# Kernel tuning notes

Measured on AMD Instinct MI355X. Metric: run time of the kernel, lower is better.

Reference implementation:

```python
import jax, jax.numpy as jnp
import numpy as np

N_HEADS = 8
WINDOW = 4

def setup_inputs() -> dict:
    key = jax.random.key(0)
    ks = jax.random.split(key, 12)
    B, C, L = 8, 512, 1024
    Dh = C // N_HEADS
    s = 1.0 / np.sqrt(C)
    inp = {
        'x': jax.random.normal(ks[0], (B, C, L), dtype=jnp.float32),
        'Wq': jax.random.normal(ks[1], (C, C), dtype=jnp.float32) * s,
        'bq': jnp.zeros((C,), dtype=jnp.float32),
        'Wk': jax.random.normal(ks[2], (C, C), dtype=jnp.float32) * s,
        'bk': jnp.zeros((C,), dtype=jnp.float32),
        'Wv': jax.random.normal(ks[3], (C, C), dtype=jnp.float32) * s,
        'bv': jnp.zeros((C,), dtype=jnp.float32),
        'Wo': jax.random.normal(ks[4], (C, C), dtype=jnp.float32) * s,
        'bo': jnp.zeros((C,), dtype=jnp.float32),
        'emb_rel_k': jax.random.normal(ks[5], (2 * WINDOW + 1, Dh), dtype=jnp.float32) * 0.02,
        'emb_rel_v': jax.random.normal(ks[6], (2 * WINDOW + 1, Dh), dtype=jnp.float32) * 0.02,
    }
    return inp


def reference(x, Wq, bq, Wk, bk, Wv, bv, Wo, bo, emb_rel_k, emb_rel_v):
    B, C, L = x.shape
    H = N_HEADS
    Dh = C // H
    scale = Dh ** -0.5

    def proj(W, b):
        # pointwise conv1d == channel-mixing matmul; (B,C,L) -> (B,H,L,Dh)
        y = jnp.einsum('oc,bcl->bol', W, x) + b[:, None]
        return y.reshape(B, H, Dh, L).transpose(0, 1, 3, 2)

    q = proj(Wq, bq) * scale
    k = proj(Wk, bk)
    v = proj(Wv, bv)

    scores = jnp.einsum('bhld,bhjd->bhlj', q, k)  # (B,H,L,L)

    t = jnp.arange(L)
    diff = t[None, :] - t[:, None]                      # (L,L)
    window_mask = (jnp.abs(diff) <= WINDOW)
    indices = jnp.clip(diff, -WINDOW, WINDOW) + WINDOW  # (L,L) in [0, 2w]

    rel_k = emb_rel_k[indices]                          # (L,L,Dh)
    rel_scores = jnp.einsum('bhld,ljd->bhlj', q, rel_k)
    scores = scores + rel_scores * window_mask[None, None, :, :]

    attn = jax.nn.softmax(scores, axis=-1)

    out = jnp.einsum('bhlj,bhjd->bhld', attn, v)
    rel_v = emb_rel_v[indices] * window_mask[:, :, None]  # (L,L,Dh)
    out = out + jnp.einsum('bhlj,ljd->bhld', attn, rel_v)

    out = out.transpose(0, 1, 3, 2).reshape(B, C, L)
    out = jnp.einsum('oc,bcl->bol', Wo, out) + bo[:, None]
    return out
```

## Files before the change

### kernel.cpp

```cpp
#include <hip/hip_runtime.h>
#include <math.h>

#define B_  8
#define H_  8
#define C_  512
#define L_  1024
#define DH  64
#define WIN 4

typedef __attribute__((ext_vector_type(8))) short short8;
typedef __attribute__((ext_vector_type(4))) float floatx4;

__device__ __forceinline__ unsigned short f2bf(float f) {
    unsigned int u = __float_as_uint(f);
    u = u + 0x7FFFu + ((u >> 16) & 1u);
    return (unsigned short)(u >> 16);
}
__device__ __forceinline__ float bf2f(unsigned short h) {
    return __uint_as_float(((unsigned int)h) << 16);
}
__device__ __forceinline__ unsigned short f2h(float f) {
    _Float16 h = (_Float16)f;
    return *reinterpret_cast<unsigned short*>(&h);
}

__global__ __launch_bounds__(256) void prep_kernel(
    const float* __restrict__ Wq, const float* __restrict__ Wk,
    const float* __restrict__ Wv, const float* __restrict__ Wo,
    const float* __restrict__ bq, const float* __restrict__ bk,
    const float* __restrict__ bv,
    unsigned short* __restrict__ Wqkv_hi,
    unsigned short* __restrict__ Wo_h,
    float* __restrict__ bqkv)
{
    const int i = blockIdx.x * 256 + threadIdx.x;
    float4 v; ushort4 h;

    v = ((const float4*)Wq)[i];
    h.x = f2bf(v.x); h.y = f2bf(v.y); h.z = f2bf(v.z); h.w = f2bf(v.w);
    ((ushort4*)Wqkv_hi)[i] = h;

    v = ((const float4*)Wk)[i];
    h.x = f2bf(v.x); h.y = f2bf(v.y); h.z = f2bf(v.z); h.w = f2bf(v.w);
    ((ushort4*)Wqkv_hi)[65536 + i] = h;

    v = ((const float4*)Wv)[i];
    h.x = f2bf(v.x); h.y = f2bf(v.y); h.z = f2bf(v.z); h.w = f2bf(v.w);
    ((ushort4*)Wqkv_hi)[131072 + i] = h;

    v = ((const float4*)Wo)[i];
    h.x = f2h(v.x); h.y = f2h(v.y); h.z = f2h(v.z); h.w = f2h(v.w);
    ((ushort4*)Wo_h)[i] = h;

    if (i < 512)       bqkv[i] = bq[i];
    else if (i < 1024) bqkv[i] = bk[i - 512];
    else if (i < 1536) bqkv[i] = bv[i - 1024];
}

__global__ __launch_bounds__(256) void transpose_kernel(
    const float* __restrict__ x, unsigned short* __restrict__ xT)
{
    __shared__ float tile[32][33];
    const int b  = blockIdx.z;
    const int cb = blockIdx.y * 32;
    const int lb = blockIdx.x * 32;
    const int t  = threadIdx.x;
    {
        const int l = t & 31, c0 = t >> 5;
#pragma unroll
        for (int p = 0; p < 4; ++p) {
            const int c = c0 + 8 * p;
            tile[c][l] = x[((size_t)b * C_ + cb + c) * L_ + lb + l];
        }
    }
    __syncthreads();
    {
        const int c = t & 31, l0 = t >> 5;
#pragma unroll
        for (int p = 0; p < 4; ++p) {
            const int l = l0 + 8 * p;
            xT[((size_t)b * L_ + lb + l) * C_ + cb + c] = f2bf(tile[c][l]);
        }
    }
}

__global__ __launch_bounds__(256) void qkv_gemm_kernel(
    const unsigned short* __restrict__ Wh, const float* __restrict__ bqkv,
    const unsigned short* __restrict__ xT,
    unsigned short* __restrict__ Qb, unsigned short* __restrict__ Kb,
    unsigned short* __restrict__ Vc)
{
    __shared__ __align__(16) unsigned short AB[2][2][128][40];

    const int b   = blockIdx.z;
    const int oB  = blockIdx.y * 128;
    const int mat = oB >> 9;
    const int ob  = oB & 511;
    const int lb  = blockIdx.x * 128;
    const int t  = threadIdx.x;
    const int w = t >> 6, lane = t & 63, quad = lane >> 4, lc = lane & 15;
    const int wm = w >> 1, wn = w & 1;

    const unsigned short* Wm = Wh + (size_t)mat * C_ * C_;

    floatx4 acc[4][4];
#pragma unroll
    for (int i = 0; i < 4; ++i)
#pragma unroll
        for (int j = 0; j < 4; ++j) acc[i][j] = (floatx4)0.f;

    const int c8 = (t & 3) * 8, r0 = t >> 2;

#pragma unroll
    for (int p = 0; p < 2; ++p) {
        *reinterpret_cast<uint4*>(&AB[0][0][r0 + 64 * p][c8]) =
            *reinterpret_cast<const uint4*>(&Wm[(size_t)(ob + r0 + 64 * p) * C_ + c8]);
        *reinterpret_cast<uint4*>(&AB[1][0][r0 + 64 * p][c8]) =
            *reinterpret_cast<const uint4*>(&xT[((size_t)b * L_ + lb + r0 + 64 * p) * C_ + c8]);
    }
    __syncthreads();

    for (int s = 0; s < 16; ++s) {
        const int cur = s & 1;

        uint4 pa[2], pb[2];
        if (s < 15) {
            const int c0n = (s + 1) * 32;
#pragma unroll
            for (int p = 0; p < 2; ++p) {
                pa[p] = *reinterpret_cast<const uint4*>(
                    &Wm[(size_t)(ob + r0 + 64 * p) * C_ + c0n + c8]);
                pb[p] = *reinterpret_cast<const uint4*>(
                    &xT[((size_t)b * L_ + lb + r0 + 64 * p) * C_ + c0n + c8]);
            }
        }

        short8 a[4], bb[4];
#pragma unroll
        for (int mt = 0; mt < 4; ++mt)
            a[mt] = *reinterpret_cast<const short8*>(
                &AB[0][cur][wm * 64 + mt * 16 + lc][quad * 8]);
#pragma unroll
        for (int nt = 0; nt < 4; ++nt)
            bb[nt] = *reinterpret_cast<const short8*>(
                &AB[1][cur][wn * 64 + nt * 16 + lc][quad * 8]);
#pragma unroll
        for (int mt = 0; mt < 4; ++mt)
#pragma unroll
            for (int nt = 0; nt < 4; ++nt)
                acc[mt][nt] = __builtin_amdgcn_mfma_f32_16x16x32_bf16(
                    a[mt], bb[nt], acc[mt][nt], 0, 0, 0);

        if (s < 15) {
#pragma unroll
            for (int p = 0; p < 2; ++p) {
                *reinterpret_cast<uint4*>(&AB[0][1 - cur][r0 + 64 * p][c8]) = pa[p];
                *reinterpret_cast<uint4*>(&AB[1][1 - cur][r0 + 64 * p][c8]) = pb[p];
            }
        }
        __syncthreads();
    }

    if (mat == 2) {
#pragma unroll
        for (int mt = 0; mt < 4; ++mt) {
#pragma unroll
            for (int r = 0; r < 4; ++r) {
                const int o  = ob + wm * 64 + mt * 16 + quad * 4 + r;
                const float bi = bqkv[1024 + o];
#pragma unroll
                for (int nt = 0; nt < 4; ++nt) {
                    const int l = lb + wn * 64 + nt * 16 + lc;
                    Vc[((size_t)b * C_ + o) * L_ + l] = f2bf(acc[mt][nt][r] + bi);
                }
            }
        }
    } else {
        const float scale = (mat == 0) ? 0.125f : 1.0f;
        unsigned short* dst = (mat == 0) ? Qb : Kb;
        unsigned short (*sT)[144] =
            reinterpret_cast<unsigned short (*)[144]>(&AB[0][0][0][0]);

#pragma unroll
        for (int mt = 0; mt < 4; ++mt) {
#pragma unroll
            for (int r = 0; r < 4; ++r) {
                const int o  = ob + wm * 64 + mt * 16 + quad * 4 + r;
                const float bi = bqkv[mat * 512 + o];
                const int d  = mt * 16 + quad * 4 + r;
#pragma unroll
                for (int nt = 0; nt < 4; ++nt) {
                    const int l = wn * 64 + nt * 16 + lc;
                    sT[l][wm * 72 + d] = f2bf((acc[mt][nt][r] + bi) * scale);
                }
            }
        }
        __syncthreads();
        {
            const int l = t >> 1, hf = t & 1;
#pragma unroll
            for (int h01 = 0; h01 < 2; ++h01) {
                const int hgl = (ob >> 6) + h01;
                const size_t o = (((size_t)b * H_ + hgl) * L_ + lb + l) * DH + hf * 32;
                const int cbase = h01 * 72 + hf * 32;
                uint4 v0 = *reinterpret_cast<const uint4*>(&sT[l][cbase]);
                uint4 v1 = *reinterpret_cast<const uint4*>(&sT[l][cbase + 8]);
                uint4 v2 = *reinterpret_cast<const uint4*>(&sT[l][cbase + 16]);
                uint4 v3 = *reinterpret_cast<const uint4*>(&sT[l][cbase + 24]);
                *reinterpret_cast<uint4*>(&dst[o])      = v0;
                *reinterpret_cast<uint4*>(&dst[o + 8])  = v1;
                *reinterpret_cast<uint4*>(&dst[o + 16]) = v2;
                *reinterpret_cast<uint4*>(&dst[o + 24]) = v3;
            }
        }
    }
}

__global__ __launch_bounds__(512, 4) void attn_kernel8(
    const unsigned short* __restrict__ Qb,
    const unsigned short* __restrict__ Kb,
    const unsigned short* __restrict__ Vc,
    const float* __restrict__ erel_k, const float* __restrict__ erel_v,
    unsigned short* __restrict__ AOh)
{
    __shared__ __align__(16) unsigned short kst[2][64][68];
    __shared__ __align__(16) unsigned short vst[2][64][68];
    __shared__ __align__(16) unsigned short Pl[8][16][68];
    __shared__ float rs[128][9];
    __shared__ float rv[128][9];

    const int t  = threadIdx.x;
    const int bh = blockIdx.x;
    const int rt = blockIdx.y;
    const int b = bh >> 3, h = bh & 7;
    const int w = t >> 6, lane = t & 63, quad = lane >> 4, lc = lane & 15;
    const int row0 = rt * 128;
    const int rowW = row0 + w * 16;

    const size_t qkBase = (size_t)bh * L_ * DH;
    const size_t vBase  = ((size_t)b * C_ + h * DH) * L_;

    for (int i = lane; i < 16 * 9; i += 64) rv[w * 16 + i / 9][i % 9] = 0.f;

    short8 af[2];
#pragma unroll
    for (int kk = 0; kk < 2; ++kk)
        af[kk] = *reinterpret_cast<const short8*>(
            &Qb[qkBase + (size_t)(rowW + lc) * DH + kk * 32 + quad * 8]);

    {
        floatx4 rsa = (floatx4)0.f;
        const int drow = (lc < 9) ? lc : 8;
#pragma unroll
        for (int kk = 0; kk < 2; ++kk) {
            short8 bfr;
#pragma unroll
            for (int i = 0; i < 8; ++i)
                bfr[i] = (short)f2bf(erel_k[drow * 64 + kk * 32 + quad * 8 + i]);
            rsa = __builtin_amdgcn_mfma_f32_16x16x32_bf16(af[kk], bfr, rsa, 0, 0, 0);
        }
        if (lc < 9) {
#pragma unroll
            for (int r = 0; r < 4; ++r)
                rs[w * 16 + quad * 4 + r][lc] = rsa[r];
        }
    }

    const int jr = t >> 3, jc = (t & 7) * 8;
    *reinterpret_cast<uint4*>(&kst[0][jr][jc]) =
        *reinterpret_cast<const uint4*>(&Kb[qkBase + (size_t)jr * DH + jc]);
    *reinterpret_cast<uint4*>(&vst[0][jr][jc]) =
        *reinterpret_cast<const uint4*>(&Vc[vBase + (size_t)jr * L_ + jc]);
    __syncthreads();

    short8 ones;
#pragma unroll
    for (int j = 0; j < 8; ++j) ones[j] = (short)0x3F80;

    floatx4 acc_o[4], acc_l = (floatx4)0.f;
#pragma unroll
    for (int nt = 0; nt < 4; ++nt) acc_o[nt] = (floatx4)0.f;

    for (int jt = 0; jt < L_ / 64; ++jt) {
        const int j0  = jt * 64;
        const int cur = jt & 1;

        uint4 pk, pv;
        if (jt < L_ / 64 - 1) {
            const int j0n = j0 + 64;
            pk = *reinterpret_cast<const uint4*>(
                &Kb[qkBase + (size_t)(j0n + jr) * DH + jc]);
            pv = *reinterpret_cast<const uint4*>(
                &Vc[vBase + (size_t)jr * L_ + j0n + jc]);
        }

        floatx4 sacc[4];
#pragma unroll
        for (int nt = 0; nt < 4; ++nt) sacc[nt] = (floatx4)0.f;
#pragma unroll
        for (int nt = 0; nt < 4; ++nt)
#pragma unroll
            for (int kk = 0; kk < 2; ++kk) {
                const short8 kf = *reinterpret_cast<const short8*>(
                    &kst[cur][nt * 16 + lc][kk * 32 + quad * 8]);
                sacc[nt] = __builtin_amdgcn_mfma_f32_16x16x32_bf16(af[kk], kf, sacc[nt], 0, 0, 0);
            }

        const bool nearD = (j0 <= rowW + 15 + WIN) && (j0 + 63 >= rowW - WIN);
        if (nearD) {
#pragma unroll
            for (int nt = 0; nt < 4; ++nt) {
                const int jg = j0 + nt * 16 + lc;
#pragma unroll
                for (int r = 0; r < 4; ++r) {
                    const int diff = jg - (rowW + quad * 4 + r);
                    if (diff >= -WIN && diff <= WIN)
                        sacc[nt][r] += rs[w * 16 + quad * 4 + r][diff + WIN];
                }
            }
        }

#pragma unroll
        for (int nt = 0; nt < 4; ++nt)
#pragma unroll
            for (int r = 0; r < 4; ++r)
                Pl[w][quad * 4 + r][nt * 16 + lc] = f2bf(__expf(sacc[nt][r]));

        if (nearD) {
            for (int idx = lane; idx < 16 * 9; idx += 64) {
                const int r16 = idx / 9, dr = idx % 9;
                const int jg = rowW + r16 + dr - WIN;
                if (jg >= j0 && jg < j0 + 64 && jg >= 0 && jg < L_)
                    rv[w * 16 + r16][dr] += bf2f(Pl[w][r16][jg - j0]);
            }
        }

        short8 pf[2];
#pragma unroll
        for (int kk = 0; kk < 2; ++kk)
            pf[kk] = *reinterpret_cast<const short8*>(&Pl[w][lc][kk * 32 + quad * 8]);

#pragma unroll
        for (int kk = 0; kk < 2; ++kk)
            acc_l = __builtin_amdgcn_mfma_f32_16x16x32_bf16(pf[kk], ones, acc_l, 0, 0, 0);

#pragma unroll
        for (int nt = 0; nt < 4; ++nt)
#pragma unroll
            for (int kk = 0; kk < 2; ++kk) {
                const short8 vf = *reinterpret_cast<const short8*>(
                    &vst[cur][nt * 16 + lc][kk * 32 + quad * 8]);
                acc_o[nt] = __builtin_amdgcn_mfma_f32_16x16x32_bf16(pf[kk], vf, acc_o[nt], 0, 0, 0);
            }

        if (jt < L_ / 64 - 1) {
            *reinterpret_cast<uint4*>(&kst[1 - cur][jr][jc]) = pk;
            *reinterpret_cast<uint4*>(&vst[1 - cur][jr][jc]) = pv;
        }
        __syncthreads();
    }

#pragma unroll
    for (int nt = 0; nt < 4; ++nt) {
        const int d = nt * 16 + lc;
        float ev[9];
#pragma unroll
        for (int dr = 0; dr < 9; ++dr) ev[dr] = erel_v[dr * 64 + d];
#pragma unroll
        for (int r = 0; r < 4; ++r) {
            const int rloc = w * 16 + quad * 4 + r;
            float v = acc_o[nt][r];
#pragma unroll
            for (int dr = 0; dr < 9; ++dr) v += rv[rloc][dr] * ev[dr];
            Pl[w][quad * 4 + r][nt * 16 + lc] = f2h(v / acc_l[r]);
        }
    }
    {
        const int row = lane >> 2, ds8 = (lane & 3) * 16;
        const uint4 q0 = *reinterpret_cast<const uint4*>(&Pl[w][row][ds8]);
        const uint4 q1 = *reinterpret_cast<const uint4*>(&Pl[w][row][ds8 + 8]);
        const size_t o = ((size_t)b * L_ + rowW + row) * C_ + h * 64 + ds8;
        *reinterpret_cast<uint4*>(&AOh[o])     = q0;
        *reinterpret_cast<uint4*>(&AOh[o + 8]) = q1;
    }
}

__global__ __launch_bounds__(256) void out_gemm_kernel(
    const unsigned short* __restrict__ Wh,
    const float* __restrict__ bo,
    const unsigned short* __restrict__ Ah,
    float* __restrict__ Y)
{
    __shared__ __align__(16) unsigned short Asb[2][128][40];
    __shared__ __align__(16) unsigned short Bsb[2][64][40];

    const int b  = blockIdx.z;
    const int ob = blockIdx.y * 128;
    const int lb = blockIdx.x * 64;
    const int t  = threadIdx.x;
    const int w = t >> 6, lane = t & 63, quad = lane >> 4, lc = lane & 15;
    const int wm = w >> 1, wn = w & 1;

    floatx4 acc[4][2];
#pragma unroll
    for (int i = 0; i < 4; ++i)
#pragma unroll
        for (int j = 0; j < 2; ++j) acc[i][j] = (floatx4)0.f;

    const int c8 = (t & 3) * 8, r0 = t >> 2;

#pragma unroll
    for (int p = 0; p < 2; ++p)
        *reinterpret_cast<uint4*>(&Asb[0][r0 + 64 * p][c8]) =
            *reinterpret_cast<const uint4*>(&Wh[(size_t)(ob + r0 + 64 * p) * C_ + c8]);
    *reinterpret_cast<uint4*>(&Bsb[0][r0][c8]) =
        *reinterpret_cast<const uint4*>(&Ah[((size_t)b * L_ + lb + r0) * C_ + c8]);
    __syncthreads();

    for (int s = 0; s < 16; ++s) {
        const int cur = s & 1;

        uint4 pa[2], pb;
        if (s < 15) {
            const int c0n = (s + 1) * 32;
#pragma unroll
            for (int p = 0; p < 2; ++p)
                pa[p] = *reinterpret_cast<const uint4*>(
                    &Wh[(size_t)(ob + r0 + 64 * p) * C_ + c0n + c8]);
            pb = *reinterpret_cast<const uint4*>(
                &Ah[((size_t)b * L_ + lb + r0) * C_ + c0n + c8]);
        }

        short8 ah[4], bhf[2];
#pragma unroll
        for (int mt = 0; mt < 4; ++mt)
            ah[mt] = *reinterpret_cast<const short8*>(
                &Asb[cur][wm * 64 + mt * 16 + lc][quad * 8]);
#pragma unroll
        for (int nt = 0; nt < 2; ++nt)
            bhf[nt] = *reinterpret_cast<const short8*>(
                &Bsb[cur][wn * 32 + nt * 16 + lc][quad * 8]);
#pragma unroll
        for (int mt = 0; mt < 4; ++mt)
#pragma unroll
            for (int nt = 0; nt < 2; ++nt)
                acc[mt][nt] = __builtin_amdgcn_mfma_f32_16x16x32_f16(
                    ah[mt], bhf[nt], acc[mt][nt], 0, 0, 0);

        if (s < 15) {
#pragma unroll
            for (int p = 0; p < 2; ++p)
                *reinterpret_cast<uint4*>(&Asb[1 - cur][r0 + 64 * p][c8]) = pa[p];
            *reinterpret_cast<uint4*>(&Bsb[1 - cur][r0][c8]) = pb;
        }
        __syncthreads();
    }

#pragma unroll
    for (int mt = 0; mt < 4; ++mt) {
#pragma unroll
        for (int r = 0; r < 4; ++r) {
            const int o = ob + wm * 64 + mt * 16 + quad * 4 + r;
            const float bi = bo[o];
#pragma unroll
            for (int nt = 0; nt < 2; ++nt) {
                const int l = lb + wn * 32 + nt * 16 + lc;
                Y[((size_t)b * C_ + o) * L_ + l] = acc[mt][nt][r] + bi;
            }
        }
    }
}

extern "C" void kernel_launch(void* const* d_in, const int* in_sizes, int n_in,
                              void* d_out, int out_size, void* d_ws, size_t ws_size,
                              hipStream_t stream)
{
    const float* x   = (const float*)d_in[0];
    const float* Wq  = (const float*)d_in[1];
    const float* bq  = (const float*)d_in[2];
    const float* Wk  = (const float*)d_in[3];
    const float* bk  = (const float*)d_in[4];
    const float* Wv  = (const float*)d_in[5];
    const float* bv  = (const float*)d_in[6];
    const float* Wo  = (const float*)d_in[7];
    const float* bo  = (const float*)d_in[8];
    const float* erk = (const float*)d_in[9];
    const float* erv = (const float*)d_in[10];

    char* ws = (char*)d_ws;
    const size_t MB = 1024u * 1024u;
    unsigned short* xT      = (unsigned short*)(ws);
    unsigned short* Qb      = (unsigned short*)(ws + 8 * MB);
    unsigned short* Kb      = (unsigned short*)(ws + 16 * MB);
    unsigned short* Vc      = (unsigned short*)(ws + 24 * MB);
    unsigned short* AOh     = (unsigned short*)(ws + 32 * MB);
    unsigned short* Wqkv_hi = (unsigned short*)(ws + 40 * MB);
    unsigned short* Wo_h    = (unsigned short*)(ws + 42 * MB);
    float*          bqkv    = (float*)(ws + 43 * MB);

    prep_kernel<<<256, 256, 0, stream>>>(Wq, Wk, Wv, Wo, bq, bk, bv,
                                         Wqkv_hi, Wo_h, bqkv);
    transpose_kernel<<<dim3(L_ / 32, C_ / 32, B_), 256, 0, stream>>>(x, xT);
    qkv_gemm_kernel<<<dim3(L_ / 128, 12, B_), 256, 0, stream>>>(
        Wqkv_hi, bqkv, xT, Qb, Kb, Vc);
    attn_kernel8<<<dim3(64, 8), 512, 0, stream>>>(
        Qb, Kb, Vc, erk, erv, AOh);
    out_gemm_kernel<<<dim3(L_ / 64, C_ / 128, B_), 256, 0, stream>>>(
        Wo_h, bo, AOh, (float*)d_out);
}
```

Before: 175.3 us.

## Process two key tiles per iteration to interleave QK and PV MFMA work

The attention main loop now handles 128 keys per iteration as two 64-key sub-tiles held in both LDS buffers. The QK product of the second sub-tile is issued between the softmax-exp and the PV product of the first, so independent MFMA work can overlap the dependent chain. Global prefetch of the next 128 keys is issued up front, and the LDS refill sits between two barriers. This raises live register pressure (two score sets plus four prefetch vectors) under a 512x4 launch bound, which risks spills or lower occupancy.

```diff
diff --git a/kernel.cpp b/kernel.cpp
--- a/kernel.cpp
+++ b/kernel.cpp
@@ -216,7 +216,7 @@
     }
 }
 
-__global__ __launch_bounds__(512, 4) void attn_kernel8(
+__global__ __launch_bounds__(512, 4) void attn_kernel9(
     const unsigned short* __restrict__ Qb,
     const unsigned short* __restrict__ Kb,
     const unsigned short* __restrict__ Vc,
@@ -271,6 +271,10 @@
         *reinterpret_cast<const uint4*>(&Kb[qkBase + (size_t)jr * DH + jc]);
     *reinterpret_cast<uint4*>(&vst[0][jr][jc]) =
         *reinterpret_cast<const uint4*>(&Vc[vBase + (size_t)jr * L_ + jc]);
+    *reinterpret_cast<uint4*>(&kst[1][jr][jc]) =
+        *reinterpret_cast<const uint4*>(&Kb[qkBase + (size_t)(64 + jr) * DH + jc]);
+    *reinterpret_cast<uint4*>(&vst[1][jr][jc]) =
+        *reinterpret_cast<const uint4*>(&Vc[vBase + (size_t)jr * L_ + 64 + jc]);
     __syncthreads();
 
     short8 ones;
@@ -281,20 +285,7 @@
 #pragma unroll
     for (int nt = 0; nt < 4; ++nt) acc_o[nt] = (floatx4)0.f;
 
-    for (int jt = 0; jt < L_ / 64; ++jt) {
-        const int j0  = jt * 64;
-        const int cur = jt & 1;
-
-        uint4 pk, pv;
-        if (jt < L_ / 64 - 1) {
-            const int j0n = j0 + 64;
-            pk = *reinterpret_cast<const uint4*>(
-                &Kb[qkBase + (size_t)(j0n + jr) * DH + jc]);
-            pv = *reinterpret_cast<const uint4*>(
-                &Vc[vBase + (size_t)jr * L_ + j0n + jc]);
-        }
-
-        floatx4 sacc[4];
+    auto qk_tile = [&](const unsigned short (*kbuf)[68], floatx4* sacc) {
 #pragma unroll
         for (int nt = 0; nt < 4; ++nt) sacc[nt] = (floatx4)0.f;
 #pragma unroll
@@ -302,10 +293,13 @@
 #pragma unroll
             for (int kk = 0; kk < 2; ++kk) {
                 const short8 kf = *reinterpret_cast<const short8*>(
-                    &kst[cur][nt * 16 + lc][kk * 32 + quad * 8]);
-                sacc[nt] = __builtin_amdgcn_mfma_f32_16x16x32_bf16(af[kk], kf, sacc[nt], 0, 0, 0);
-            }
-
+                    &kbuf[nt * 16 + lc][kk * 32 + quad * 8]);
+                sacc[nt] = __builtin_amdgcn_mfma_f32_16x16x32_bf16(
+                    af[kk], kf, sacc[nt], 0, 0, 0);
+            }
+    };
+
+    auto expw_tile = [&](int j0, floatx4* sacc) {
         const bool nearD = (j0 <= rowW + 15 + WIN) && (j0 + 63 >= rowW - WIN);
         if (nearD) {
 #pragma unroll
@@ -319,13 +313,11 @@
                 }
             }
         }
-
 #pragma unroll
         for (int nt = 0; nt < 4; ++nt)
 #pragma unroll
             for (int r = 0; r < 4; ++r)
                 Pl[w][quad * 4 + r][nt * 16 + lc] = f2bf(__expf(sacc[nt][r]));
-
         if (nearD) {
             for (int idx = lane; idx < 16 * 9; idx += 64) {
                 const int r16 = idx / 9, dr = idx % 9;
@@ -334,30 +326,59 @@
                     rv[w * 16 + r16][dr] += bf2f(Pl[w][r16][jg - j0]);
             }
         }
-
+    };
+
+    auto pv_tile = [&](const unsigned short (*vbuf)[68]) {
         short8 pf[2];
 #pragma unroll
         for (int kk = 0; kk < 2; ++kk)
             pf[kk] = *reinterpret_cast<const short8*>(&Pl[w][lc][kk * 32 + quad * 8]);
-
 #pragma unroll
         for (int kk = 0; kk < 2; ++kk)
             acc_l = __builtin_amdgcn_mfma_f32_16x16x32_bf16(pf[kk], ones, acc_l, 0, 0, 0);
-
 #pragma unroll
         for (int nt = 0; nt < 4; ++nt)
 #pragma unroll
             for (int kk = 0; kk < 2; ++kk) {
                 const short8 vf = *reinterpret_cast<const short8*>(
-                    &vst[cur][nt * 16 + lc][kk * 32 + quad * 8]);
-                acc_o[nt] = __builtin_amdgcn_mfma_f32_16x16x32_bf16(pf[kk], vf, acc_o[nt], 0, 0, 0);
-            }
-
-        if (jt < L_ / 64 - 1) {
-            *reinterpret_cast<uint4*>(&kst[1 - cur][jr][jc]) = pk;
-            *reinterpret_cast<uint4*>(&vst[1 - cur][jr][jc]) = pv;
-        }
-        __syncthreads();
+                    &vbuf[nt * 16 + lc][kk * 32 + quad * 8]);
+                acc_o[nt] = __builtin_amdgcn_mfma_f32_16x16x32_bf16(
+                    pf[kk], vf, acc_o[nt], 0, 0, 0);
+            }
+    };
+
+    for (int p = 0; p < 8; ++p) {
+        const int j00 = p * 128;
+        const int j01 = j00 + 64;
+
+        uint4 pk0, pv0, pk1, pv1;
+        if (p < 7) {
+            pk0 = *reinterpret_cast<const uint4*>(
+                &Kb[qkBase + (size_t)(j00 + 128 + jr) * DH + jc]);
+            pv0 = *reinterpret_cast<const uint4*>(
+                &Vc[vBase + (size_t)jr * L_ + j00 + 128 + jc]);
+            pk1 = *reinterpret_cast<const uint4*>(
+                &Kb[qkBase + (size_t)(j00 + 192 + jr) * DH + jc]);
+            pv1 = *reinterpret_cast<const uint4*>(
+                &Vc[vBase + (size_t)jr * L_ + j00 + 192 + jc]);
+        }
+
+        floatx4 s0[4], s1[4];
+        qk_tile(kst[0], s0);
+        expw_tile(j00, s0);
+        qk_tile(kst[1], s1);
+        pv_tile(vst[0]);
+        expw_tile(j01, s1);
+        pv_tile(vst[1]);
+
+        if (p < 7) {
+            __syncthreads();
+            *reinterpret_cast<uint4*>(&kst[0][jr][jc]) = pk0;
+            *reinterpret_cast<uint4*>(&vst[0][jr][jc]) = pv0;
+            *reinterpret_cast<uint4*>(&kst[1][jr][jc]) = pk1;
+            *reinterpret_cast<uint4*>(&vst[1][jr][jc]) = pv1;
+            __syncthreads();
+        }
     }
 
 #pragma unroll
@@ -503,7 +524,7 @@
     transpose_kernel<<<dim3(L_ / 32, C_ / 32, B_), 256, 0, stream>>>(x, xT);
     qkv_gemm_kernel<<<dim3(L_ / 128, 12, B_), 256, 0, stream>>>(
         Wqkv_hi, bqkv, xT, Qb, Kb, Vc);
-    attn_kernel8<<<dim3(64, 8), 512, 0, stream>>>(
+    attn_kernel9<<<dim3(64, 8), 512, 0, stream>>>(
         Qb, Kb, Vc, erk, erv, AOh);
     out_gemm_kernel<<<dim3(L_ / 64, C_ / 128, B_), 256, 0, stream>>>(
         Wo_h, bo, AOh, (float*)d_out);
```

Result: slower. 263.8 us (+50.5%).
